# Optimization experiments

Hardware: AMD Instinct MI355X
Metric: run time of the kernel (lower is better)

Reference implementation:

```python
import jax, jax.numpy as jnp
import numpy as np

BS, V, J = 256, 10475, 55
NSHAPE, NEXP = 300, 50

# SMPLX kinematic tree (fixed model constant)
PARENTS = np.array([
    -1, 0, 0, 0, 1, 2, 3, 4, 5, 6, 7, 8, 9, 9, 9, 12, 13, 14, 16, 17, 18, 19,
    15, 15, 15,
    20, 25, 26, 20, 28, 29, 20, 31, 32, 20, 34, 35, 20, 37, 38,
    21, 40, 41, 21, 43, 44, 21, 46, 47, 21, 49, 50, 21, 52, 53], dtype=np.int64)


def batch_rodrigues(rvec):
    # rvec: [N,3] axis-angle -> [N,3,3] rotation matrices
    angle = jnp.linalg.norm(rvec + 1e-8, axis=-1, keepdims=True)  # [N,1]
    axis = rvec / angle
    x, y, z = axis[..., 0], axis[..., 1], axis[..., 2]
    zr = jnp.zeros_like(x)
    K = jnp.stack([zr, -z, y, z, zr, -x, -y, x, zr], axis=-1).reshape(-1, 3, 3)
    s = jnp.sin(angle)[..., None]
    c = jnp.cos(angle)[..., None]
    I = jnp.eye(3, dtype=rvec.dtype)
    return I + s * K + (1.0 - c) * (K @ K)


def setup_inputs():
    key = jax.random.key(0)
    ks = jax.random.split(key, 9)
    pose = 0.2 * jax.random.normal(ks[0], (BS, 53, 3), jnp.float32)
    shape = jax.random.normal(ks[1], (BS, 10), jnp.float32)
    expression = jax.random.normal(ks[2], (BS, NEXP), jnp.float32)
    global_orient = 0.2 * jax.random.normal(ks[3], (1, 3), jnp.float32)
    v_template = jax.random.normal(ks[4], (V, 3), jnp.float32)
    shapedirs = 0.01 * jax.random.normal(ks[5], (V, 3, NSHAPE + NEXP), jnp.float32)
    posedirs = 0.01 * jax.random.normal(ks[6], (486, V * 3), jnp.float32)
    J_regressor = jax.random.uniform(ks[7], (J, V), jnp.float32)
    J_regressor = J_regressor / jnp.sum(J_regressor, axis=1, keepdims=True)
    lbs_weights = jax.random.uniform(ks[8], (V, J), jnp.float32)
    lbs_weights = lbs_weights / jnp.sum(lbs_weights, axis=1, keepdims=True)
    return {"pose": pose, "shape": shape, "expression": expression,
            "global_orient": global_orient, "v_template": v_template,
            "shapedirs": shapedirs, "posedirs": posedirs,
            "J_regressor": J_regressor, "lbs_weights": lbs_weights}


def lbs(betas, rot_mats, v_template, shapedirs, posedirs, J_regressor, lbs_weights):
    bs = betas.shape[0]
    dt = betas.dtype
    # shape blendshapes
    v_shaped = v_template[None] + jnp.einsum('bl,vcl->bvc', betas, shapedirs)
    # rest-pose joints
    joints = jnp.einsum('jv,bvc->bjc', J_regressor, v_shaped)  # [b,J,3]
    # pose blendshapes
    I3 = jnp.eye(3, dtype=dt)
    pose_feature = (rot_mats[:, 1:] - I3).reshape(bs, -1)  # [b,(J-1)*9]
    v_posed = v_shaped + jnp.einsum('bp,pn->bn', pose_feature, posedirs).reshape(bs, V, 3)
    # forward kinematics along the tree
    rel_joints = jnp.concatenate(
        [joints[:, :1], joints[:, 1:] - joints[:, PARENTS[1:]]], axis=1)
    top = jnp.concatenate([rot_mats, rel_joints[..., None]], axis=-1)  # [b,J,3,4]
    bot = jnp.broadcast_to(jnp.array([0, 0, 0, 1], dtype=dt), (bs, J, 1, 4))
    T_local = jnp.concatenate([top, bot], axis=-2)  # [b,J,4,4]
    A_list = [T_local[:, 0]]
    for j in range(1, J):  # fixed 55-joint chain
        A_list.append(A_list[int(PARENTS[j])] @ T_local[:, j])
    A = jnp.stack(A_list, axis=1)  # [b,J,4,4]
    posed_joints = A[..., :3, 3]
    # subtract rest-pose contribution
    corr = jnp.einsum('bjmn,bjn->bjm', A[..., :3, :3], joints)
    A_rel = A.at[..., :3, 3].add(-corr)
    # vertex skinning
    T = jnp.einsum('vj,bjmn->bvmn', lbs_weights, A_rel)  # [b,V,4,4]
    verts = jnp.einsum('bvmn,bvn->bvm', T[..., :3, :3], v_posed) + T[..., :3, 3]
    return verts, posed_joints


def reference(pose, shape, expression, global_orient, v_template, shapedirs,
              posedirs, J_regressor, lbs_weights):
    bs = pose.shape[0]
    dt = pose.dtype
    go = jnp.broadcast_to(global_orient[:, None, :], (bs, 1, 3))
    eyes = jnp.zeros((bs, 2, 3), dtype=dt)  # leye/reye fixed at zero
    # order: global, body(21), jaw, leye, reye, lhand(15), rhand(15) -> 55
    full_pose = jnp.concatenate(
        [go, pose[:, 1:22], pose[:, 52:53], eyes, pose[:, 22:37], pose[:, 37:52]],
        axis=1)
    betas = jnp.concatenate(
        [shape, jnp.zeros((bs, NSHAPE - shape.shape[1]), dtype=dt), expression],
        axis=1)  # [b,350]
    rot_mats = batch_rodrigues(full_pose.reshape(-1, 3)).reshape(bs, J, 3, 3)
    verts, joints = lbs(betas, rot_mats, v_template, shapedirs, posedirs,
                        J_regressor, lbs_weights)
    return verts, joints
```

## Files before the change

### kernel.cpp

```cpp
#include <hip/hip_runtime.h>
#include <math.h>

#define BS 256
#define V 10475
#define NJ 55
#define R3 31425
#define NP 486
#define LB 60
#define KP 576
#define VK 10496
#define JOFF 8044800
#define NKSPLIT 164

#define NB_POSE 56
#define NB_JREGB 2624
#define NB_TRX 164
#define NB_WB 656
#define NB_TRD 4428
#define B0_JREGB (NB_POSE)
#define B0_TRX (B0_JREGB + NB_JREGB)
#define B0_WB (B0_TRX + NB_TRX)
#define B0_TRD (B0_WB + NB_WB)
#define NB_PRE (B0_TRD + NB_TRD)

typedef __attribute__((ext_vector_type(8))) short short8;
typedef __attribute__((ext_vector_type(4))) float float4_;

__device__ const int PARENTS_d[NJ] = {
  -1, 0, 0, 0, 1, 2, 3, 4, 5, 6, 7, 8, 9, 9, 9, 12, 13, 14, 16, 17, 18, 19,
  15, 15, 15, 20, 25, 26, 20, 28, 29, 20, 31, 32, 20, 34, 35, 20, 37, 38,
  21, 40, 41, 21, 43, 44, 21, 46, 47, 21, 49, 50, 21, 52, 53
};

__device__ __forceinline__ unsigned short f2b(float f) {
  unsigned int u = __float_as_uint(f);
  unsigned int r = (u + 0x7FFFu + ((u >> 16) & 1u)) >> 16;
  return (unsigned short)r;
}

__global__ __launch_bounds__(256) void k_pre(
    const float* __restrict__ pose, const float* __restrict__ shp,
    const float* __restrict__ expr, const float* __restrict__ go,
    const float* __restrict__ Jreg, const float* __restrict__ lbs,
    const float* __restrict__ sd, const float* __restrict__ vt,
    const float* __restrict__ pd,
    float* __restrict__ rot_ws, unsigned short* __restrict__ Ftr,
    float* __restrict__ betas_T, unsigned short* __restrict__ Jregb,
    unsigned short* __restrict__ Wb, unsigned short* __restrict__ XbT,
    unsigned short* __restrict__ Dtr) {
  __shared__ float smem[64 * 68];
  int blk = blockIdx.x;
  int t = threadIdx.x;

  if (blk < NB_POSE) {
    int b = t;
    int j = blk;
    if (j == NJ) {
      #pragma unroll
      for (int l = 0; l < 10; ++l) {
        float v = shp[b * 10 + l];
        betas_T[l * BS + b] = v;
        Ftr[(size_t)b * KP + NP + l] = f2b(v);
      }
      #pragma unroll
      for (int l = 0; l < 50; ++l) {
        float v = expr[b * 50 + l];
        betas_T[(10 + l) * BS + b] = v;
        Ftr[(size_t)b * KP + NP + 10 + l] = f2b(v);
      }
      #pragma unroll
      for (int l = NP + LB; l < KP; ++l) Ftr[(size_t)b * KP + l] = 0;
      return;
    }
    float rx, ry, rz;
    if (j == 0) { rx = go[0]; ry = go[1]; rz = go[2]; }
    else if (j == 23 || j == 24) { rx = 0.f; ry = 0.f; rz = 0.f; }
    else {
      int src = (j <= 21) ? j : (j == 22 ? 52 : j - 3);
      const float* p = pose + ((size_t)b * 53 + src) * 3;
      rx = p[0]; ry = p[1]; rz = p[2];
    }
    float sx = rx + 1e-8f, sy = ry + 1e-8f, sz = rz + 1e-8f;
    float ang = sqrtf(sx * sx + sy * sy + sz * sz);
    float inv = 1.f / ang;
    float x = rx * inv, y = ry * inv, z = rz * inv;
    float s = sinf(ang), c = cosf(ang), C = 1.f - c;
    float R[9];
    R[0] = 1.f - C * (y * y + z * z);
    R[1] = -s * z + C * x * y;
    R[2] =  s * y + C * x * z;
    R[3] =  s * z + C * x * y;
    R[4] = 1.f - C * (x * x + z * z);
    R[5] = -s * x + C * y * z;
    R[6] = -s * y + C * x * z;
    R[7] =  s * x + C * y * z;
    R[8] = 1.f - C * (x * x + y * y);
    float* rw = rot_ws + ((size_t)b * NJ + j) * 9;
    #pragma unroll
    for (int e = 0; e < 9; ++e) rw[e] = R[e];
    if (j >= 1) {
      int pb = (j - 1) * 9;
      #pragma unroll
      for (int e = 0; e < 9; ++e)
        Ftr[(size_t)b * KP + pb + e] =
            f2b(R[e] - ((e == 0 || e == 4 || e == 8) ? 1.f : 0.f));
    }
  } else if (blk < B0_TRX) {
    size_t idx = (size_t)(blk - B0_JREGB) * 256 + t;
    int j = (int)(idx / VK);
    int v = (int)(idx - (size_t)j * VK);
    float val = (j < NJ && v < V) ? Jreg[(size_t)j * V + v] : 0.f;
    Jregb[idx] = f2b(val);
  } else if (blk < B0_WB) {
    int v0 = (blk - B0_TRX) * 64;
    #pragma unroll 1
    for (int c = 0; c < 3; ++c) {
      for (int idx = t; idx < 3840; idx += 256) {
        int v_l = idx / 60, col = idx - v_l * 60;
        int v = v0 + v_l;
        int cidx = (col < 10) ? col : 290 + col;
        smem[col * 65 + v_l] = (v < V) ? sd[((size_t)v * 3 + c) * 350 + cidx] : 0.f;
      }
      {
        int v_l = t & 63, rr = t >> 6;
        int v = v0 + v_l;
        smem[(60 + rr) * 65 + v_l] =
            (rr == 0 && v < V) ? vt[(size_t)v * 3 + c] : 0.f;
      }
      __syncthreads();
      for (int idx = t; idx < 4096; idx += 256) {
        int cl = idx >> 6, v_l = idx & 63;
        XbT[(size_t)(c * 64 + cl) * VK + v0 + v_l] = f2b(smem[cl * 65 + v_l]);
      }
      __syncthreads();
    }
  } else if (blk < B0_TRD) {
    int v0 = (blk - B0_WB) * 16;
    for (int idx = t; idx < 1024; idx += 256) {
      int v_l = idx >> 6, k = idx & 63;
      int v = v0 + v_l;
      float val = (k < NJ && v < V) ? lbs[(size_t)v * NJ + k] : 0.f;
      if (v < VK) Wb[(size_t)v * 64 + k] = f2b(val);
    }
  } else {
    int b2 = blk - B0_TRD;
    int rt = b2 % 492, kt = b2 / 492;
    int r0 = rt * 64;
    int c = (t & 15) * 4;
    #pragma unroll
    for (int s = 0; s < 4; ++s) {
      int k_l = (t >> 4) + 16 * s;
      int kg = kt * 64 + k_l;
      float v0 = 0.f, v1 = 0.f, v2 = 0.f, v3 = 0.f;
      int r = r0 + c;
      if (kg < NP) {
        if (r + 3 < R3) {
          const float* p = pd + (size_t)kg * R3 + r;
          v0 = p[0]; v1 = p[1]; v2 = p[2]; v3 = p[3];
        } else {
          const float* p = pd + (size_t)kg * R3;
          if (r < R3)     v0 = p[r];
          if (r + 1 < R3) v1 = p[r + 1];
          if (r + 2 < R3) v2 = p[r + 2];
          if (r + 3 < R3) v3 = p[r + 3];
        }
      } else if (kg < NP + LB) {
        int ll = kg - NP;
        int cidx = (ll < 10) ? ll : (290 + ll);
        if (r < R3)     v0 = sd[(size_t)(r) * 350 + cidx];
        if (r + 1 < R3) v1 = sd[(size_t)(r + 1) * 350 + cidx];
        if (r + 2 < R3) v2 = sd[(size_t)(r + 2) * 350 + cidx];
        if (r + 3 < R3) v3 = sd[(size_t)(r + 3) * 350 + cidx];
      }
      float* tp = smem + k_l * 68 + c;
      tp[0] = v0; tp[1] = v1; tp[2] = v2; tp[3] = v3;
    }
    __syncthreads();
    int r_l = t >> 2, a = t & 3;
    unsigned short h[16];
    #pragma unroll
    for (int i = 0; i < 16; ++i) h[i] = f2b(smem[(a * 16 + i) * 68 + r_l]);
    unsigned short* dp = Dtr + (size_t)(r0 + r_l) * KP + kt * 64 + a * 16;
    #pragma unroll
    for (int i = 0; i < 16; ++i) dp[i] = h[i];
  }
}

__global__ __launch_bounds__(256) void k_jsm(
    const unsigned short* __restrict__ Jregb,
    const unsigned short* __restrict__ XbT, float* __restrict__ Ppart) {
  int lane = threadIdx.x & 63;
  int wv = threadIdx.x >> 6;
  int l15 = lane & 15, q = lane >> 4;
  int k0 = blockIdx.x * 64;
  const unsigned short* ap = Jregb + (size_t)(wv * 16 + l15) * VK + k0 + q * 8;
  float4_ acc[12];
  #pragma unroll
  for (int nt = 0; nt < 12; ++nt) acc[nt] = (float4_)0.f;
  #pragma unroll
  for (int ks = 0; ks < 2; ++ks) {
    short8 a = *(const short8*)(ap + ks * 32);
    #pragma unroll
    for (int nt = 0; nt < 12; ++nt) {
      const unsigned short* bp =
          XbT + (size_t)(nt * 16 + l15) * VK + k0 + ks * 32 + q * 8;
      short8 b = *(const short8*)bp;
      acc[nt] = __builtin_amdgcn_mfma_f32_16x16x32_bf16(a, b, acc[nt], 0, 0, 0);
    }
  }
  float* pp = Ppart + (size_t)blockIdx.x * 10080;
  #pragma unroll
  for (int nt = 0; nt < 12; ++nt) {
    int cl = nt * 16 + l15;
    int c = cl >> 6, l = cl & 63;
    if (l < 61) {
      #pragma unroll
      for (int reg = 0; reg < 4; ++reg) {
        int jj = wv * 16 + q * 4 + reg;
        if (jj < NJ) pp[((size_t)jj * 3 + c) * 61 + l] = acc[nt][reg];
      }
    }
  }
}

__global__ __launch_bounds__(256) void k_jsred(
    const float* __restrict__ Ppart, float* __restrict__ JS) {
  int idx = blockIdx.x * 256 + threadIdx.x;
  if (idx >= 10065) return;
  float s = 0.f;
  #pragma unroll 4
  for (int p = 0; p < NKSPLIT; ++p) s += Ppart[(size_t)p * 10080 + idx];
  JS[idx] = s;
}

__global__ __launch_bounds__(64) void k_chain(
    const float* __restrict__ JS, const float* __restrict__ betas_T,
    const float* __restrict__ rot_ws, unsigned short* __restrict__ arelb,
    float* __restrict__ out) {
  int b = blockIdx.x;
  int lane = threadIdx.x;
  __shared__ float joints_l[165];
  __shared__ float Tl[880];
  __shared__ float A[880];
  for (int idx = lane; idx < 165; idx += 64) {
    float sacc = JS[idx * 61 + 60];
    #pragma unroll
    for (int l = 0; l < LB; ++l) sacc += JS[idx * 61 + l] * betas_T[l * BS + b];
    joints_l[idx] = sacc;
  }
  __syncthreads();
  for (int idx = lane; idx < 880; idx += 64) {
    int j = idx >> 4, e = idx & 15, r = e >> 2, cc = e & 3;
    float val;
    if (r < 3) {
      if (cc < 3) val = rot_ws[((size_t)b * NJ + j) * 9 + r * 3 + cc];
      else {
        int par = PARENTS_d[j];
        val = joints_l[j * 3 + r] - (par >= 0 ? joints_l[par * 3 + r] : 0.f);
      }
    } else val = (cc == 3) ? 1.f : 0.f;
    Tl[idx] = val;
  }
  __syncthreads();
  if (lane < 16) A[lane] = Tl[lane];
  __syncthreads();
  for (int j = 1; j < NJ; ++j) {
    int par = PARENTS_d[j];
    if (lane < 16) {
      int r = lane >> 2, cc = lane & 3;
      float sacc = 0.f;
      #pragma unroll
      for (int k = 0; k < 4; ++k)
        sacc += A[par * 16 + r * 4 + k] * Tl[j * 16 + k * 4 + cc];
      A[j * 16 + lane] = sacc;
    }
    __syncthreads();
  }
  for (int idx = lane; idx < 165; idx += 64) {
    int j = idx / 3, r = idx % 3;
    out[JOFF + (size_t)b * 165 + idx] = A[j * 16 + r * 4 + 3];
  }
  for (int idx = lane; idx < 1024; idx += 64) {
    int n = idx >> 6, k = idx & 63;
    float val = 0.f;
    if (n < 12 && k < NJ) {
      int m = n >> 2, cc = n & 3;
      if (cc < 3) val = A[k * 16 + m * 4 + cc];
      else {
        val = A[k * 16 + m * 4 + 3]
            - (A[k * 16 + m * 4 + 0] * joints_l[k * 3 + 0] +
               A[k * 16 + m * 4 + 1] * joints_l[k * 3 + 1] +
               A[k * 16 + m * 4 + 2] * joints_l[k * 3 + 2]);
      }
    }
    arelb[(size_t)b * 1024 + idx] = f2b(val);
  }
}

__global__ __launch_bounds__(256) void k_gemm(
    const float* __restrict__ vt, const unsigned short* __restrict__ Ftr,
    const unsigned short* __restrict__ Dtr, float* __restrict__ out) {
  int lane = threadIdx.x & 63;
  int wv = threadIdx.x >> 6;
  int l15 = lane & 15, q = lane >> 4;
  int r0 = blockIdx.x * 64;
  int m0 = wv * 64;
  float4_ acc[4][4];
  #pragma unroll
  for (int mt = 0; mt < 4; ++mt)
    #pragma unroll
    for (int nt = 0; nt < 4; ++nt) acc[mt][nt] = (float4_)0.f;

  const unsigned short* aBase[4];
  const unsigned short* bBase[4];
  #pragma unroll
  for (int mt = 0; mt < 4; ++mt)
    aBase[mt] = Ftr + (size_t)(m0 + mt * 16 + l15) * KP + q * 8;
  #pragma unroll
  for (int nt = 0; nt < 4; ++nt)
    bBase[nt] = Dtr + (size_t)(r0 + nt * 16 + l15) * KP + q * 8;

  short8 af[4], bf[4], an[4], bn[4];
  #pragma unroll
  for (int mt = 0; mt < 4; ++mt) af[mt] = *(const short8*)(aBase[mt]);
  #pragma unroll
  for (int nt = 0; nt < 4; ++nt) bf[nt] = *(const short8*)(bBase[nt]);

  #pragma unroll 1
  for (int kk = 0; kk < 18; ++kk) {
    if (kk < 17) {
      int off = (kk + 1) * 32;
      #pragma unroll
      for (int mt = 0; mt < 4; ++mt) an[mt] = *(const short8*)(aBase[mt] + off);
      #pragma unroll
      for (int nt = 0; nt < 4; ++nt) bn[nt] = *(const short8*)(bBase[nt] + off);
    }
    #pragma unroll
    for (int mt = 0; mt < 4; ++mt)
      #pragma unroll
      for (int nt = 0; nt < 4; ++nt)
        acc[mt][nt] = __builtin_amdgcn_mfma_f32_16x16x32_bf16(
            af[mt], bf[nt], acc[mt][nt], 0, 0, 0);
    #pragma unroll
    for (int mt = 0; mt < 4; ++mt) af[mt] = an[mt];
    #pragma unroll
    for (int nt = 0; nt < 4; ++nt) bf[nt] = bn[nt];
  }

  #pragma unroll
  for (int nt = 0; nt < 4; ++nt) {
    int r = r0 + nt * 16 + l15;
    if (r < R3) {
      float vtv = vt[r];
      #pragma unroll
      for (int mt = 0; mt < 4; ++mt) {
        int bb = m0 + mt * 16 + q * 4;
        #pragma unroll
        for (int reg = 0; reg < 4; ++reg)
          out[(size_t)(bb + reg) * R3 + r] = acc[mt][nt][reg] + vtv;
      }
    }
  }
}

__global__ __launch_bounds__(256) void k_skin(
    const unsigned short* __restrict__ Wb, const unsigned short* __restrict__ arelb,
    float* __restrict__ out) {
  int lane = threadIdx.x & 63;
  int wv = threadIdx.x >> 6;
  int l15 = lane & 15, q = lane >> 4;
  int v0w = blockIdx.x * 64 + wv * 16;
  int b0 = blockIdx.y * 16;

  const unsigned short* wp = Wb + (size_t)(v0w + l15) * 64 + q * 8;
  short8 w0 = *(const short8*)(wp);
  short8 w1 = *(const short8*)(wp + 32);

  int vi = lane / 3;
  int ci = lane - vi * 3;
  int srcT = ci * 16 + (vi & 15);
  int srcX = vi * 3 <= 63 ? vi * 3 : 63;
  int r = v0w * 3 + lane;
  bool rok = (lane < 48) && (r < R3);

  float vload = 0.f;
  if (rok) vload = out[(size_t)b0 * R3 + r];
  const unsigned short* ap = arelb + (size_t)b0 * 1024 + l15 * 64 + q * 8;
  short8 a0 = *(const short8*)ap;
  short8 a1 = *(const short8*)(ap + 32);

  #pragma unroll 1
  for (int bi = 0; bi < 16; ++bi) {
    int b = b0 + bi;
    float nvload = 0.f;
    short8 na0 = a0, na1 = a1;
    if (bi < 15) {
      if (rok) nvload = out[(size_t)(b + 1) * R3 + r];
      const unsigned short* np = arelb + (size_t)(b + 1) * 1024 + l15 * 64 + q * 8;
      na0 = *(const short8*)np;
      na1 = *(const short8*)(np + 32);
    }
    float4_ acc = (float4_)0.f;
    acc = __builtin_amdgcn_mfma_f32_16x16x32_bf16(a0, w0, acc, 0, 0, 0);
    acc = __builtin_amdgcn_mfma_f32_16x16x32_bf16(a1, w1, acc, 0, 0, 0);
    float T0 = __shfl(acc[0], srcT, 64);
    float T1 = __shfl(acc[1], srcT, 64);
    float T2 = __shfl(acc[2], srcT, 64);
    float T3 = __shfl(acc[3], srcT, 64);
    float x = __shfl(vload, srcX, 64);
    float y = __shfl(vload, srcX + 1 <= 63 ? srcX + 1 : 63, 64);
    float z = __shfl(vload, srcX + 2 <= 63 ? srcX + 2 : 63, 64);
    if (rok) out[(size_t)b * R3 + r] = T0 * x + T1 * y + T2 * z + T3;
    vload = nvload; a0 = na0; a1 = na1;
  }
}

extern "C" void kernel_launch(void* const* d_in, const int* in_sizes, int n_in,
                              void* d_out, int out_size, void* d_ws, size_t ws_size,
                              hipStream_t stream) {
  const float* pose = (const float*)d_in[0];
  const float* shp  = (const float*)d_in[1];
  const float* expr = (const float*)d_in[2];
  const float* go   = (const float*)d_in[3];
  const float* vt   = (const float*)d_in[4];
  const float* sd   = (const float*)d_in[5];
  const float* pd   = (const float*)d_in[6];
  const float* jr   = (const float*)d_in[7];
  const float* lbs  = (const float*)d_in[8];
  float* out = (float*)d_out;
  float* ws  = (float*)d_ws;

  float* betas_T        = ws;
  float* rot_ws         = ws + 15360;
  float* JS             = ws + 142080;
  unsigned short* Ftr   = (unsigned short*)(ws + 152160);
  unsigned short* arelb = (unsigned short*)(ws + 225888);
  unsigned short* Wb    = (unsigned short*)(ws + 356960);
  unsigned short* Jregb = (unsigned short*)(ws + 692832);
  unsigned short* XbT   = (unsigned short*)(ws + 1028704);
  unsigned short* Dtr   = (unsigned short*)(ws + 2036320);
  float* Ppart          = ws + 11104864;

  k_pre<<<NB_PRE, 256, 0, stream>>>(pose, shp, expr, go, jr, lbs, sd, vt, pd,
                                    rot_ws, Ftr, betas_T, Jregb, Wb, XbT, Dtr);
  k_jsm<<<NKSPLIT, 256, 0, stream>>>(Jregb, XbT, Ppart);
  k_jsred<<<40, 256, 0, stream>>>(Ppart, JS);
  k_chain<<<BS, 64, 0, stream>>>(JS, betas_T, rot_ws, arelb, out);
  k_gemm<<<492, 256, 0, stream>>>(vt, Ftr, Dtr, out);
  k_skin<<<dim3(164, 16), 256, 0, stream>>>(Wb, arelb, out);
}
```

Before: 296.4 us.

## Fuse posed-vertex GEMM with skinning through shared memory slab

Merges the blendshape GEMM and the skinning kernel into one kernel. Each block now computes 48 rows (16 vertices × 3 coords) for all 256 batches, keeps the posed vertices in an LDS slab, and skins them right away. This removes the full write-then-reread of posed vertices through global memory and one kernel launch. In exchange the tiles are narrower (3 n-tiles instead of 4), each wave runs a serial 64-batch skin loop, and the launch has more blocks with a larger LDS footprint.

```diff
diff --git a/kernel.cpp b/kernel.cpp
--- a/kernel.cpp
+++ b/kernel.cpp
@@ -11,6 +11,7 @@
 #define VK 10496
 #define JOFF 8044800
 #define NKSPLIT 164
+#define VPP 67
 
 #define NB_POSE 56
 #define NB_JREGB 2624
@@ -297,34 +298,40 @@
   }
 }
 
-__global__ __launch_bounds__(256) void k_gemm(
+__global__ __launch_bounds__(256) void k_gs(
     const float* __restrict__ vt, const unsigned short* __restrict__ Ftr,
-    const unsigned short* __restrict__ Dtr, float* __restrict__ out) {
+    const unsigned short* __restrict__ Dtr,
+    const unsigned short* __restrict__ Wb,
+    const unsigned short* __restrict__ arelb, float* __restrict__ out) {
+  __shared__ float vpw[4][48 * VPP];
   int lane = threadIdx.x & 63;
   int wv = threadIdx.x >> 6;
   int l15 = lane & 15, q = lane >> 4;
-  int r0 = blockIdx.x * 64;
+  int r0 = blockIdx.x * 48;
+  int v0 = blockIdx.x * 16;
   int m0 = wv * 64;
-  float4_ acc[4][4];
+  float* slab = &vpw[wv][0];
+
+  float4_ acc[4][3];
   #pragma unroll
   for (int mt = 0; mt < 4; ++mt)
     #pragma unroll
-    for (int nt = 0; nt < 4; ++nt) acc[mt][nt] = (float4_)0.f;
+    for (int nt = 0; nt < 3; ++nt) acc[mt][nt] = (float4_)0.f;
 
   const unsigned short* aBase[4];
-  const unsigned short* bBase[4];
+  const unsigned short* bBase[3];
   #pragma unroll
   for (int mt = 0; mt < 4; ++mt)
     aBase[mt] = Ftr + (size_t)(m0 + mt * 16 + l15) * KP + q * 8;
   #pragma unroll
-  for (int nt = 0; nt < 4; ++nt)
+  for (int nt = 0; nt < 3; ++nt)
     bBase[nt] = Dtr + (size_t)(r0 + nt * 16 + l15) * KP + q * 8;
 
-  short8 af[4], bf[4], an[4], bn[4];
+  short8 af[4], bf[3], an[4], bn[3];
   #pragma unroll
   for (int mt = 0; mt < 4; ++mt) af[mt] = *(const short8*)(aBase[mt]);
   #pragma unroll
-  for (int nt = 0; nt < 4; ++nt) bf[nt] = *(const short8*)(bBase[nt]);
+  for (int nt = 0; nt < 3; ++nt) bf[nt] = *(const short8*)(bBase[nt]);
 
   #pragma unroll 1
   for (int kk = 0; kk < 18; ++kk) {
@@ -333,85 +340,62 @@
       #pragma unroll
       for (int mt = 0; mt < 4; ++mt) an[mt] = *(const short8*)(aBase[mt] + off);
       #pragma unroll
-      for (int nt = 0; nt < 4; ++nt) bn[nt] = *(const short8*)(bBase[nt] + off);
+      for (int nt = 0; nt < 3; ++nt) bn[nt] = *(const short8*)(bBase[nt] + off);
     }
     #pragma unroll
     for (int mt = 0; mt < 4; ++mt)
       #pragma unroll
-      for (int nt = 0; nt < 4; ++nt)
+      for (int nt = 0; nt < 3; ++nt)
         acc[mt][nt] = __builtin_amdgcn_mfma_f32_16x16x32_bf16(
             af[mt], bf[nt], acc[mt][nt], 0, 0, 0);
     #pragma unroll
     for (int mt = 0; mt < 4; ++mt) af[mt] = an[mt];
     #pragma unroll
-    for (int nt = 0; nt < 4; ++nt) bf[nt] = bn[nt];
-  }
-
-  #pragma unroll
-  for (int nt = 0; nt < 4; ++nt) {
+    for (int nt = 0; nt < 3; ++nt) bf[nt] = bn[nt];
+  }
+
+  #pragma unroll
+  for (int nt = 0; nt < 3; ++nt) {
     int r = r0 + nt * 16 + l15;
-    if (r < R3) {
-      float vtv = vt[r];
-      #pragma unroll
-      for (int mt = 0; mt < 4; ++mt) {
-        int bb = m0 + mt * 16 + q * 4;
-        #pragma unroll
-        for (int reg = 0; reg < 4; ++reg)
-          out[(size_t)(bb + reg) * R3 + r] = acc[mt][nt][reg] + vtv;
-      }
-    }
-  }
-}
-
-__global__ __launch_bounds__(256) void k_skin(
-    const unsigned short* __restrict__ Wb, const unsigned short* __restrict__ arelb,
-    float* __restrict__ out) {
-  int lane = threadIdx.x & 63;
-  int wv = threadIdx.x >> 6;
-  int l15 = lane & 15, q = lane >> 4;
-  int v0w = blockIdx.x * 64 + wv * 16;
-  int b0 = blockIdx.y * 16;
-
-  const unsigned short* wp = Wb + (size_t)(v0w + l15) * 64 + q * 8;
+    float vtv = (r < R3) ? vt[r] : 0.f;
+    #pragma unroll
+    for (int mt = 0; mt < 4; ++mt)
+      #pragma unroll
+      for (int reg = 0; reg < 4; ++reg)
+        slab[(nt * 16 + l15) * VPP + mt * 16 + q * 4 + reg] =
+            acc[mt][nt][reg] + vtv;
+  }
+
+  const unsigned short* wp = Wb + (size_t)(v0 + l15) * 64 + q * 8;
   short8 w0 = *(const short8*)(wp);
   short8 w1 = *(const short8*)(wp + 32);
-
-  int vi = lane / 3;
-  int ci = lane - vi * 3;
-  int srcT = ci * 16 + (vi & 15);
-  int srcX = vi * 3 <= 63 ? vi * 3 : 63;
-  int r = v0w * 3 + lane;
-  bool rok = (lane < 48) && (r < R3);
-
-  float vload = 0.f;
-  if (rok) vload = out[(size_t)b0 * R3 + r];
-  const unsigned short* ap = arelb + (size_t)b0 * 1024 + l15 * 64 + q * 8;
+  int v = v0 + l15;
+  bool vok = (q < 3) && (v < V);
+  size_t obase = (size_t)v * 3 + q;
+
+  const unsigned short* ap = arelb + (size_t)m0 * 1024 + l15 * 64 + q * 8;
   short8 a0 = *(const short8*)ap;
   short8 a1 = *(const short8*)(ap + 32);
 
   #pragma unroll 1
-  for (int bi = 0; bi < 16; ++bi) {
-    int b = b0 + bi;
-    float nvload = 0.f;
+  for (int bi = 0; bi < 64; ++bi) {
+    int b = m0 + bi;
     short8 na0 = a0, na1 = a1;
-    if (bi < 15) {
-      if (rok) nvload = out[(size_t)(b + 1) * R3 + r];
+    if (bi < 63) {
       const unsigned short* np = arelb + (size_t)(b + 1) * 1024 + l15 * 64 + q * 8;
       na0 = *(const short8*)np;
       na1 = *(const short8*)(np + 32);
     }
-    float4_ acc = (float4_)0.f;
-    acc = __builtin_amdgcn_mfma_f32_16x16x32_bf16(a0, w0, acc, 0, 0, 0);
-    acc = __builtin_amdgcn_mfma_f32_16x16x32_bf16(a1, w1, acc, 0, 0, 0);
-    float T0 = __shfl(acc[0], srcT, 64);
-    float T1 = __shfl(acc[1], srcT, 64);
-    float T2 = __shfl(acc[2], srcT, 64);
-    float T3 = __shfl(acc[3], srcT, 64);
-    float x = __shfl(vload, srcX, 64);
-    float y = __shfl(vload, srcX + 1 <= 63 ? srcX + 1 : 63, 64);
-    float z = __shfl(vload, srcX + 2 <= 63 ? srcX + 2 : 63, 64);
-    if (rok) out[(size_t)b * R3 + r] = T0 * x + T1 * y + T2 * z + T3;
-    vload = nvload; a0 = na0; a1 = na1;
+    float x = slab[(l15 * 3 + 0) * VPP + bi];
+    float y = slab[(l15 * 3 + 1) * VPP + bi];
+    float z = slab[(l15 * 3 + 2) * VPP + bi];
+    float4_ sacc = (float4_)0.f;
+    sacc = __builtin_amdgcn_mfma_f32_16x16x32_bf16(a0, w0, sacc, 0, 0, 0);
+    sacc = __builtin_amdgcn_mfma_f32_16x16x32_bf16(a1, w1, sacc, 0, 0, 0);
+    if (vok)
+      out[(size_t)b * R3 + obase] =
+          sacc[0] * x + sacc[1] * y + sacc[2] * z + sacc[3];
+    a0 = na0; a1 = na1;
   }
 }
 
@@ -446,6 +430,5 @@
   k_jsm<<<NKSPLIT, 256, 0, stream>>>(Jregb, XbT, Ppart);
   k_jsred<<<40, 256, 0, stream>>>(Ppart, JS);
   k_chain<<<BS, 64, 0, stream>>>(JS, betas_T, rot_ws, arelb, out);
-  k_gemm<<<492, 256, 0, stream>>>(vt, Ftr, Dtr, out);
-  k_skin<<<dim3(164, 16), 256, 0, stream>>>(Wb, arelb, out);
-}
+  k_gs<<<655, 256, 0, stream>>>(vt, Ftr, Dtr, Wb, arelb, out);
+}
```

After: 299.0 us. No clear change (+0.9%).
